# Performance work log

Hardware: AMD Instinct MI355X
Metric: run time of the kernel (lower is better)

Reference implementation:

```python
import jax, jax.numpy as jnp
import numpy as np

CODEBOOK_NUM = 8192
CODEBOOK_DIM = 256
BETA = 1.0


def setup_inputs() -> dict:
    key = jax.random.key(0)
    k1, k2 = jax.random.split(key)
    z = jax.random.normal(k1, (8, CODEBOOK_DIM, 16, 16, 16), dtype=jnp.float32)
    # torch init: uniform_(-1/codebook_num, 1/codebook_num)
    codebook = jax.random.uniform(
        k2, (CODEBOOK_NUM, CODEBOOK_DIM), dtype=jnp.float32,
        minval=-1.0 / CODEBOOK_NUM, maxval=1.0 / CODEBOOK_NUM)
    return {"z": z, "codebook": codebook}


def reference(z, codebook):
    # z: [B, C, D, H, W] -> [B, D, H, W, C]
    zp = jnp.transpose(z, (0, 2, 3, 4, 1))
    z_flat = zp.reshape(-1, codebook.shape[1])  # [N, C]
    # squared euclidean distances via ||a||^2 + ||b||^2 - 2 a.b
    d = (jnp.sum(z_flat ** 2, axis=1, keepdims=True)
         + jnp.sum(codebook ** 2, axis=1)
         - 2.0 * jnp.matmul(z_flat, codebook.T))  # [N, K]
    idx = jnp.argmin(d, axis=1)  # [N]
    z_q = codebook[idx].reshape(zp.shape)  # [B, D, H, W, C]
    sg = jax.lax.stop_gradient
    loss = jnp.mean((sg(z_q) - zp) ** 2) + BETA * jnp.mean((z_q - sg(zp)) ** 2)
    # straight-through estimator
    z_q_st = zp + sg(z_q - zp)
    out = jnp.transpose(z_q_st, (0, 4, 1, 2, 3))  # back to [B, C, D, H, W]
    return out, loss, idx
```

## Files before the change

kernel.cpp:

```cpp
#include <hip/hip_runtime.h>
#include <hip/hip_bf16.h>
#include <stdint.h>
#include <stddef.h>

typedef unsigned short ushort_t;
typedef unsigned int uint_t;

typedef __attribute__((ext_vector_type(8))) short short8;
typedef __attribute__((ext_vector_type(4))) float floatx4;
typedef __attribute__((ext_vector_type(16))) float floatx16;
typedef __attribute__((ext_vector_type(4))) uint_t uintx4;

#define N_ROWS 32768
#define K_ENT  8192
#define CDIM   256
#define OUT_ELEMS 8388608
#define LOSS_OFF  8388608
#define IDX_OFF   8388609
#define CAP_Q  44
#define MARGIN    2.0e-4f

__device__ __forceinline__ ushort_t f2bf(float f) {
    uint_t x = __float_as_uint(f);
    uint_t r = (x + 0x7fffu + ((x >> 16) & 1u)) >> 16;
    return (ushort_t)r;
}


__device__ __forceinline__ void gload_lds16(const ushort_t* g, ushort_t* s) {
    __builtin_amdgcn_global_load_lds(
        (__attribute__((address_space(1))) void*)(g),
        (__attribute__((address_space(3))) void*)(s), 16, 0, 0);
}

__global__ __launch_bounds__(256) void k_prep(const float* __restrict__ zin,
                                              const float* __restrict__ cb,
                                              ushort_t* __restrict__ zsw,
                                              ushort_t* __restrict__ cbsw,
                                              float* __restrict__ ztf,
                                              float* __restrict__ cn) {
    int bid = blockIdx.x;
    if (bid >= 2048) {
        int t = (bid - 2048) * 256 + threadIdx.x;
        int ent = t >> 5;
        int c0  = (t & 31) << 3;
        const float* p = cb + (size_t)ent * CDIM + c0;
        floatx4 f0 = *(const floatx4*)p;
        floatx4 f1 = *(const floatx4*)(p + 4);
        uintx4 pk;
        pk[0] = (uint_t)f2bf(f0[0]) | ((uint_t)f2bf(f0[1]) << 16);
        pk[1] = (uint_t)f2bf(f0[2]) | ((uint_t)f2bf(f0[3]) << 16);
        pk[2] = (uint_t)f2bf(f1[0]) | ((uint_t)f2bf(f1[1]) << 16);
        pk[3] = (uint_t)f2bf(f1[2]) | ((uint_t)f2bf(f1[3]) << 16);
        int idx = (ent >> 5) * 8192 + (c0 >> 4) * 512 + ((c0 >> 3) & 1) * 256 + (ent & 31) * 8;
        *(uintx4*)(cbsw + idx) = pk;
        float pn = 0.f;
#pragma unroll
        for (int qq = 0; qq < 4; ++qq) pn = fmaf(f0[qq], f0[qq], pn);
#pragma unroll
        for (int qq = 0; qq < 4; ++qq) pn = fmaf(f1[qq], f1[qq], pn);
#pragma unroll
        for (int m = 1; m < 32; m <<= 1) pn += __shfl_xor(pn, m);
        if ((t & 31) == 0) cn[ent] = pn;
        return;
    }
    __shared__ float lds[64][65];
    int c0 = (bid & 3) << 6;
    int s0 = ((bid >> 2) & 63) << 6;
    int b  = bid >> 8;
    int tid = threadIdx.x;
    int j = tid & 63, ib = tid >> 6;
    const float* zb = zin + ((size_t)b << 20);
#pragma unroll
    for (int rr = 0; rr < 16; ++rr) {
        int i = rr * 4 + ib;
        lds[i][j] = zb[(size_t)(c0 + i) * 4096 + s0 + j];
    }
    __syncthreads();
#pragma unroll
    for (int it = 0; it < 2; ++it) {
        int item = it * 256 + tid;
        int sl = item >> 3;
        int ch = item & 7;
        int row = (b << 12) + s0 + sl;
        int cg  = c0 + ch * 8;
        uintx4 pk;
        floatx4 f0, f1;
#pragma unroll
        for (int q = 0; q < 4; ++q) {
            float a = lds[ch * 8 + 2 * q][sl];
            float bqv = lds[ch * 8 + 2 * q + 1][sl];
            pk[q] = (uint_t)f2bf(a) | ((uint_t)f2bf(bqv) << 16);
        }
#pragma unroll
        for (int q = 0; q < 4; ++q) {
            f0[q] = lds[ch * 8 + q][sl];
            f1[q] = lds[ch * 8 + 4 + q][sl];
        }
        int idx = (row >> 5) * 8192 + (cg >> 4) * 512 + ((cg >> 3) & 1) * 256 + (row & 31) * 8;
        *(uintx4*)(zsw + idx) = pk;
        if (ztf) {
            *(floatx4*)(ztf + (size_t)row * 256 + cg) = f0;
            *(floatx4*)(ztf + (size_t)row * 256 + cg + 4) = f1;
        }
    }
}

__device__ __forceinline__ void screen_emit(const floatx16& acc, float& rmx,
                                            int& cur, int hi, int2* slist,
                                            int ent0) {
    float t0 = fmaxf(fmaxf(acc[0], acc[1]), fmaxf(acc[2], acc[3]));
    float t1 = fmaxf(fmaxf(acc[4], acc[5]), fmaxf(acc[6], acc[7]));
    float t2 = fmaxf(fmaxf(acc[8], acc[9]), fmaxf(acc[10], acc[11]));
    float t3 = fmaxf(fmaxf(acc[12], acc[13]), fmaxf(acc[14], acc[15]));
    float mxo = fmaxf(fmaxf(t0, t1), fmaxf(t2, t3));
    float mx = fmaxf(mxo, __shfl_xor(mxo, 32));
    float rm = fmaxf(rmx, mx);
    rmx = rm;
    float thr = rm - MARGIN;
    if (__any(mxo >= thr)) {
        uint_t mask = 0u;
#pragma unroll
        for (int r = 0; r < 16; ++r)
            if (acc[r] >= thr) mask |= (1u << r);
        int p  = __popc(mask);
        int pp = __shfl_xor(p, 32);
        int s  = cur + (hi ? pp : 0);
        cur += p + pp;
        if (mask) {
#pragma unroll
            for (int r = 0; r < 16; ++r) {
                if (mask & (1u << r)) {
                    if (s < CAP_Q)
                        slist[s] = make_int2(ent0 + (r & 3) + 8 * (r >> 2),
                                             __float_as_int(acc[r]));
                    ++s;
                }
            }
        }
    }
}

__global__ __launch_bounds__(256, 4) void k_screen(const ushort_t* __restrict__ zsw,
                                                   const ushort_t* __restrict__ cbsw,
                                                   int2* __restrict__ surv,
                                                   int* __restrict__ cnt) {
    __shared__ ushort_t bt[2][8192];
    int tid = threadIdx.x;
    int w = tid >> 6, l = tid & 63;
    int bid = blockIdx.x;
    int q  = bid & 3;
    int RB = (bid >> 2) * 128;
    int n = RB + w * 32 + (l & 31);
    int cidx = n * 4 + q;
    int2* slist = surv + (size_t)cidx * CAP_Q;
    int tile0 = q * 64;
    int hi = l & 32;

    const ushort_t* gsp = cbsw + (size_t)tile0 * 8192 + tid * 8;
    auto stage = [&](ushort_t* ld) {
#pragma unroll
        for (int j = 0; j < 4; ++j)
            gload_lds16(gsp + j * 2048, ld + j * 2048);
        gsp += 8192;
    };

    stage(&bt[0][w * 512]);

    short8 zfr[16];
    {
        const ushort_t* pz = zsw + (size_t)((RB >> 5) + w) * 8192 + l * 8;
#pragma unroll
        for (int s = 0; s < 16; ++s)
            zfr[s] = *(const short8*)(pz + s * 512);
    }
    __syncthreads();

    float rmx = -3.0e38f;
    int cur = 0;
    int esub = (l >> 5) * 4;

    floatx16 zacc;
#pragma unroll
    for (int i = 0; i < 16; ++i) zacc[i] = 0.f;

    floatx16 accA, accB;
    auto compute = [&](floatx16& acc, int b) {
        const ushort_t* bb = &bt[b][l * 8];
        short8 a0 = *(const short8*)(bb);
        acc = __builtin_amdgcn_mfma_f32_32x32x16_bf16(a0, zfr[0], zacc, 0, 0, 0);
#pragma unroll
        for (int s = 1; s < 16; ++s) {
            short8 a = *(const short8*)(bb + s * 512);
            acc = __builtin_amdgcn_mfma_f32_32x32x16_bf16(a, zfr[s], acc, 0, 0, 0);
        }
    };
    auto ent_of = [&](int t) { return (tile0 + t) * 32 + esub; };

    stage(&bt[1][w * 512]);
    __builtin_amdgcn_s_setprio(1);
    compute(accA, 0);
    __builtin_amdgcn_s_setprio(0);
    __syncthreads();

    for (int t = 1; t < 63; t += 2) {
        stage(&bt[0][w * 512]);
        __builtin_amdgcn_s_setprio(1);
        compute(accB, 1);
        screen_emit(accA, rmx, cur, hi, slist, ent_of(t - 1));
        __builtin_amdgcn_s_setprio(0);
        __syncthreads();
        stage(&bt[1][w * 512]);
        __builtin_amdgcn_s_setprio(1);
        compute(accA, 0);
        screen_emit(accB, rmx, cur, hi, slist, ent_of(t));
        __builtin_amdgcn_s_setprio(0);
        __syncthreads();
    }
    __builtin_amdgcn_s_setprio(1);
    compute(accB, 1);
    screen_emit(accA, rmx, cur, hi, slist, ent_of(62));
    __builtin_amdgcn_s_setprio(0);
    screen_emit(accB, rmx, cur, hi, slist, ent_of(63));

    if (!hi) cnt[cidx] = cur;
}

__global__ __launch_bounds__(256) void k_refine(const float* __restrict__ zin,
                                                const float* __restrict__ ztf,
                                                const float* __restrict__ cb,
                                                const int2* __restrict__ surv,
                                                const int* __restrict__ cnt,
                                                int* __restrict__ idxi,
                                                float* __restrict__ idxf,
                                                const float* __restrict__ cn,
                                                float* __restrict__ lossp) {
    __shared__ float zr[4][256];
    __shared__ float lossw[4];
    int w = threadIdx.x >> 6, l = threadIdx.x & 63;
    int n = blockIdx.x * 4 + w;
    if (ztf) {
        const float* zrow = ztf + (size_t)n * 256;
#pragma unroll
        for (int i = 0; i < 4; ++i)
            zr[w][l + 64 * i] = zrow[l + 64 * i];
    } else {
        int b = n >> 12, s = n & 4095;
        const float* zb = zin + ((size_t)b << 20) + s;
#pragma unroll
        for (int i = 0; i < 4; ++i)
            zr[w][l + 64 * i] = zb[(size_t)(l + 64 * i) << 12];
    }
    __syncthreads();
    const float* z = zr[w];
    float zn = 0.f;
    for (int c = 0; c < 256; ++c) zn = fmaf(z[c], z[c], zn);

    int c0 = cnt[n * 4 + 0], c1 = cnt[n * 4 + 1];
    int c2 = cnt[n * 4 + 2], c3 = cnt[n * 4 + 3];
    int m = c0 + c1 + c2 + c3;
    bool ok = (c0 <= CAP_Q) && (c1 <= CAP_Q) && (c2 <= CAP_Q) && (c3 <= CAP_Q) && (m >= 1);
    float bu = 3.0e38f;
    int bk = 0x7fffffff;
    if (ok) {
        int myk[3]; float myv[3]; int nc = 0;
        float vmax = -3.0e38f;
        for (int i = l; i < m; i += 64) {
            int qq, s;
            if (i < c0)            { qq = 0; s = i; }
            else if (i < c0 + c1)  { qq = 1; s = i - c0; }
            else if (i < c0 + c1 + c2) { qq = 2; s = i - c0 - c1; }
            else                   { qq = 3; s = i - c0 - c1 - c2; }
            int2 kv = surv[(n * 4 + qq) * CAP_Q + s];
            myk[nc] = kv.x;
            myv[nc] = __int_as_float(kv.y);
            vmax = fmaxf(vmax, myv[nc]);
            ++nc;
        }
#pragma unroll
        for (int msk = 1; msk < 64; msk <<= 1)
            vmax = fmaxf(vmax, __shfl_xor(vmax, msk));
        float fthr = vmax - MARGIN;
        for (int jj = 0; jj < nc; ++jj) {
            if (myv[jj] >= fthr) {
                int k = myk[jj];
                const float* cr = cb + (size_t)k * 256;
                float d = 0.f;
                for (int c = 0; c < 256; c += 4) {
                    floatx4 wv = *(const floatx4*)(cr + c);
                    d = fmaf(z[c], wv[0], d);
                    d = fmaf(z[c + 1], wv[1], d);
                    d = fmaf(z[c + 2], wv[2], d);
                    d = fmaf(z[c + 3], wv[3], d);
                }
                float u = zn - 2.0f * d;
                if (u < bu || (u == bu && k < bk)) { bu = u; bk = k; }
            }
        }
    } else {
        for (int kb = l; kb < K_ENT; kb += 256) {
            const float* p0 = cb + (size_t)(kb)       * 256;
            const float* p1 = cb + (size_t)(kb + 64)  * 256;
            const float* p2 = cb + (size_t)(kb + 128) * 256;
            const float* p3 = cb + (size_t)(kb + 192) * 256;
            float d0 = 0.f, d1 = 0.f, d2 = 0.f, d3 = 0.f;
            for (int c = 0; c < 256; c += 4) {
                floatx4 w0 = *(const floatx4*)(p0 + c);
                floatx4 w1 = *(const floatx4*)(p1 + c);
                floatx4 w2 = *(const floatx4*)(p2 + c);
                floatx4 w3 = *(const floatx4*)(p3 + c);
#pragma unroll
                for (int j = 0; j < 4; ++j) {
                    d0 = fmaf(z[c + j], w0[j], d0);
                    d1 = fmaf(z[c + j], w1[j], d1);
                    d2 = fmaf(z[c + j], w2[j], d2);
                    d3 = fmaf(z[c + j], w3[j], d3);
                }
            }
            float u0 = zn - 2.0f * d0, u1 = zn - 2.0f * d1;
            float u2 = zn - 2.0f * d2, u3 = zn - 2.0f * d3;
            if (u0 < bu) { bu = u0; bk = kb; }
            if (u1 < bu) { bu = u1; bk = kb + 64; }
            if (u2 < bu) { bu = u2; bk = kb + 128; }
            if (u3 < bu) { bu = u3; bk = kb + 192; }
        }
    }
#pragma unroll
    for (int msk = 1; msk < 64; msk <<= 1) {
        float ou = __shfl_xor(bu, msk);
        int   ok2 = __shfl_xor(bk, msk);
        if (ou < bu || (ou == bu && ok2 < bk)) { bu = ou; bk = ok2; }
    }
    if (l == 0) {
        idxi[n] = bk;
        idxf[n] = (float)bk;
        lossw[w] = bu + cn[bk];
    }
    __syncthreads();
    if (threadIdx.x == 0)
        lossp[blockIdx.x] = (lossw[0] + lossw[1]) + (lossw[2] + lossw[3]);
}

__global__ __launch_bounds__(256) void k_gather(const float* __restrict__ cb,
                                                const int* __restrict__ idxi,
                                                const float* __restrict__ lossp,
                                                float* __restrict__ out) {
    __shared__ float tile[64][65];
    __shared__ int lk[64];
    __shared__ double dsum[4];
    int t = threadIdx.x;
    int blk = blockIdx.x;
    int b = blk >> 6;
    int s0 = (blk & 63) << 6;
    int n0 = (b << 12) + s0;
    if (t < 64) lk[t] = idxi[n0 + t];
    __syncthreads();
    int wv = t >> 6, ln = t & 63;
    float* ob = out + ((size_t)b << 20);
#pragma unroll
    for (int ct = 0; ct < 4; ++ct) {
        int c0 = ct << 6;
#pragma unroll
        for (int i = 0; i < 16; ++i) {
            int sl = (wv << 4) + i;
            tile[sl][ln] = cb[(size_t)lk[sl] * 256 + c0 + ln];
        }
        __syncthreads();
#pragma unroll
        for (int j = 0; j < 16; ++j) {
            int cl = (wv << 4) + j;
            ob[(size_t)(c0 + cl) * 4096 + s0 + ln] = tile[ln][cl];
        }
        __syncthreads();
    }
    if (blk == 0) {
        double s = 0.0;
        for (int i = t; i < 8192; i += 256) s += (double)lossp[i];
#pragma unroll
        for (int msk = 1; msk < 64; msk <<= 1) s += __shfl_xor(s, msk);
        if (ln == 0) dsum[wv] = s;
        __syncthreads();
        if (t == 0)
            out[LOSS_OFF] = (float)(2.0 * ((dsum[0] + dsum[1]) + (dsum[2] + dsum[3]))
                                    / 8388608.0);
    }
}

extern "C" void kernel_launch(void* const* d_in, const int* in_sizes, int n_in,
                              void* d_out, int out_size, void* d_ws, size_t ws_size,
                              hipStream_t stream) {
    (void)in_sizes; (void)n_in; (void)out_size;
    const float* z  = (const float*)d_in[0];
    const float* cb = (const float*)d_in[1];
    float* out = (float*)d_out;
    char* ws = (char*)d_ws;

    size_t off = 0;
    ushort_t* zsw  = (ushort_t*)(ws + off); off += 16777216;
    ushort_t* cbsw = (ushort_t*)(ws + off); off += 4194304;
    float* ztf = nullptr;
    const size_t ZTF_BYTES = 33554432;
    const size_t SURV_BYTES = (size_t)N_ROWS * 4 * CAP_Q * 8;
    const size_t TAIL = SURV_BYTES + 524288 + 131072 + 32768 + 32768;
    if (ws_size >= off + ZTF_BYTES + TAIL) { ztf = (float*)(ws + off); off += ZTF_BYTES; }
    int2* surv = (int2*)(ws + off); off += SURV_BYTES;
    int* cnt    = (int*)(ws + off); off += 524288;
    int* idxi   = (int*)(ws + off); off += 131072;
    float* cn   = (float*)(ws + off); off += 32768;
    float* lossp = (float*)(ws + off); off += 32768;

    k_prep<<<3072, 256, 0, stream>>>(z, cb, zsw, cbsw, ztf, cn);
    k_screen<<<1024, 256, 0, stream>>>(zsw, cbsw, surv, cnt);
    k_refine<<<8192, 256, 0, stream>>>(z, ztf, cb, surv, cnt, idxi, out + IDX_OFF, cn, lossp);
    k_gather<<<8192 / 16, 256, 0, stream>>>(cb, idxi, lossp, out);
}
```

Measured before the change: 336.2 us.

## Fuse refine and gather kernels, drop fp32 transposed z copy

Merges the per-row refine kernel and the gather/transpose kernel into one kernel. Each block loads a 64-row z tile into LDS straight from the NCDHW input, refines those rows, then writes the gathered codebook rows back transposed. The 32 MB fp32 transposed z buffer and the separate index and loss-partial buffers go away. The loss is reduced with double atomics plus a last-block counter instead of a final pass. The risk is lower parallelism in refine: 512 blocks, each running 16 rows serially per wave, instead of 8192 blocks, and any fallback full scan now stalls a whole block.

```diff
diff --git a/kernel.cpp b/kernel.cpp
--- a/kernel.cpp
+++ b/kernel.cpp
@@ -37,11 +37,13 @@
                                               const float* __restrict__ cb,
                                               ushort_t* __restrict__ zsw,
                                               ushort_t* __restrict__ cbsw,
-                                              float* __restrict__ ztf,
-                                              float* __restrict__ cn) {
+                                              float* __restrict__ cn,
+                                              double* __restrict__ acc,
+                                              int* __restrict__ cnt2) {
     int bid = blockIdx.x;
     if (bid >= 2048) {
         int t = (bid - 2048) * 256 + threadIdx.x;
+        if (t == 0) { *acc = 0.0; *cnt2 = 0; }
         int ent = t >> 5;
         int c0  = (t & 31) << 3;
         const float* p = cb + (size_t)ent * CDIM + c0;
@@ -85,24 +87,14 @@
         int row = (b << 12) + s0 + sl;
         int cg  = c0 + ch * 8;
         uintx4 pk;
-        floatx4 f0, f1;
 #pragma unroll
         for (int q = 0; q < 4; ++q) {
             float a = lds[ch * 8 + 2 * q][sl];
             float bqv = lds[ch * 8 + 2 * q + 1][sl];
             pk[q] = (uint_t)f2bf(a) | ((uint_t)f2bf(bqv) << 16);
         }
-#pragma unroll
-        for (int q = 0; q < 4; ++q) {
-            f0[q] = lds[ch * 8 + q][sl];
-            f1[q] = lds[ch * 8 + 4 + q][sl];
-        }
         int idx = (row >> 5) * 8192 + (cg >> 4) * 512 + ((cg >> 3) & 1) * 256 + (row & 31) * 8;
         *(uintx4*)(zsw + idx) = pk;
-        if (ztf) {
-            *(floatx4*)(ztf + (size_t)row * 256 + cg) = f0;
-            *(floatx4*)(ztf + (size_t)row * 256 + cg + 4) = f1;
-        }
     }
 }
 
@@ -226,170 +218,167 @@
     if (!hi) cnt[cidx] = cur;
 }
 
-__global__ __launch_bounds__(256) void k_refine(const float* __restrict__ zin,
-                                                const float* __restrict__ ztf,
+__global__ __launch_bounds__(256) void k_refgat(const float* __restrict__ zin,
                                                 const float* __restrict__ cb,
                                                 const int2* __restrict__ surv,
                                                 const int* __restrict__ cnt,
-                                                int* __restrict__ idxi,
-                                                float* __restrict__ idxf,
                                                 const float* __restrict__ cn,
-                                                float* __restrict__ lossp) {
-    __shared__ float zr[4][256];
+                                                float* __restrict__ out,
+                                                double* __restrict__ acc,
+                                                int* __restrict__ cnt2) {
+    __shared__ float zr[64][257];
+    __shared__ int lk[64];
     __shared__ float lossw[4];
-    int w = threadIdx.x >> 6, l = threadIdx.x & 63;
-    int n = blockIdx.x * 4 + w;
-    if (ztf) {
-        const float* zrow = ztf + (size_t)n * 256;
-#pragma unroll
-        for (int i = 0; i < 4; ++i)
-            zr[w][l + 64 * i] = zrow[l + 64 * i];
-    } else {
-        int b = n >> 12, s = n & 4095;
-        const float* zb = zin + ((size_t)b << 20) + s;
-#pragma unroll
-        for (int i = 0; i < 4; ++i)
-            zr[w][l + 64 * i] = zb[(size_t)(l + 64 * i) << 12];
-    }
-    __syncthreads();
-    const float* z = zr[w];
-    float zn = 0.f;
-    for (int c = 0; c < 256; ++c) zn = fmaf(z[c], z[c], zn);
-
-    int c0 = cnt[n * 4 + 0], c1 = cnt[n * 4 + 1];
-    int c2 = cnt[n * 4 + 2], c3 = cnt[n * 4 + 3];
-    int m = c0 + c1 + c2 + c3;
-    bool ok = (c0 <= CAP_Q) && (c1 <= CAP_Q) && (c2 <= CAP_Q) && (c3 <= CAP_Q) && (m >= 1);
-    float bu = 3.0e38f;
-    int bk = 0x7fffffff;
-    if (ok) {
-        int myk[3]; float myv[3]; int nc = 0;
-        float vmax = -3.0e38f;
-        for (int i = l; i < m; i += 64) {
-            int qq, s;
-            if (i < c0)            { qq = 0; s = i; }
-            else if (i < c0 + c1)  { qq = 1; s = i - c0; }
-            else if (i < c0 + c1 + c2) { qq = 2; s = i - c0 - c1; }
-            else                   { qq = 3; s = i - c0 - c1 - c2; }
-            int2 kv = surv[(n * 4 + qq) * CAP_Q + s];
-            myk[nc] = kv.x;
-            myv[nc] = __int_as_float(kv.y);
-            vmax = fmaxf(vmax, myv[nc]);
-            ++nc;
-        }
-#pragma unroll
-        for (int msk = 1; msk < 64; msk <<= 1)
-            vmax = fmaxf(vmax, __shfl_xor(vmax, msk));
-        float fthr = vmax - MARGIN;
-        for (int jj = 0; jj < nc; ++jj) {
-            if (myv[jj] >= fthr) {
-                int k = myk[jj];
-                const float* cr = cb + (size_t)k * 256;
-                float d = 0.f;
-                for (int c = 0; c < 256; c += 4) {
-                    floatx4 wv = *(const floatx4*)(cr + c);
-                    d = fmaf(z[c], wv[0], d);
-                    d = fmaf(z[c + 1], wv[1], d);
-                    d = fmaf(z[c + 2], wv[2], d);
-                    d = fmaf(z[c + 3], wv[3], d);
-                }
-                float u = zn - 2.0f * d;
-                if (u < bu || (u == bu && k < bk)) { bu = u; bk = k; }
-            }
-        }
-    } else {
-        for (int kb = l; kb < K_ENT; kb += 256) {
-            const float* p0 = cb + (size_t)(kb)       * 256;
-            const float* p1 = cb + (size_t)(kb + 64)  * 256;
-            const float* p2 = cb + (size_t)(kb + 128) * 256;
-            const float* p3 = cb + (size_t)(kb + 192) * 256;
-            float d0 = 0.f, d1 = 0.f, d2 = 0.f, d3 = 0.f;
-            for (int c = 0; c < 256; c += 4) {
-                floatx4 w0 = *(const floatx4*)(p0 + c);
-                floatx4 w1 = *(const floatx4*)(p1 + c);
-                floatx4 w2 = *(const floatx4*)(p2 + c);
-                floatx4 w3 = *(const floatx4*)(p3 + c);
-#pragma unroll
-                for (int j = 0; j < 4; ++j) {
-                    d0 = fmaf(z[c + j], w0[j], d0);
-                    d1 = fmaf(z[c + j], w1[j], d1);
-                    d2 = fmaf(z[c + j], w2[j], d2);
-                    d3 = fmaf(z[c + j], w3[j], d3);
-                }
-            }
-            float u0 = zn - 2.0f * d0, u1 = zn - 2.0f * d1;
-            float u2 = zn - 2.0f * d2, u3 = zn - 2.0f * d3;
-            if (u0 < bu) { bu = u0; bk = kb; }
-            if (u1 < bu) { bu = u1; bk = kb + 64; }
-            if (u2 < bu) { bu = u2; bk = kb + 128; }
-            if (u3 < bu) { bu = u3; bk = kb + 192; }
-        }
-    }
-#pragma unroll
-    for (int msk = 1; msk < 64; msk <<= 1) {
-        float ou = __shfl_xor(bu, msk);
-        int   ok2 = __shfl_xor(bk, msk);
-        if (ou < bu || (ou == bu && ok2 < bk)) { bu = ou; bk = ok2; }
-    }
-    if (l == 0) {
-        idxi[n] = bk;
-        idxf[n] = (float)bk;
-        lossw[w] = bu + cn[bk];
-    }
-    __syncthreads();
-    if (threadIdx.x == 0)
-        lossp[blockIdx.x] = (lossw[0] + lossw[1]) + (lossw[2] + lossw[3]);
-}
-
-__global__ __launch_bounds__(256) void k_gather(const float* __restrict__ cb,
-                                                const int* __restrict__ idxi,
-                                                const float* __restrict__ lossp,
-                                                float* __restrict__ out) {
-    __shared__ float tile[64][65];
-    __shared__ int lk[64];
-    __shared__ double dsum[4];
     int t = threadIdx.x;
+    int wq = t >> 6, l = t & 63;
     int blk = blockIdx.x;
     int b = blk >> 6;
     int s0 = (blk & 63) << 6;
     int n0 = (b << 12) + s0;
-    if (t < 64) lk[t] = idxi[n0 + t];
+    const float* zb = zin + ((size_t)b << 20);
+
+#pragma unroll
+    for (int k = 0; k < 16; ++k) {
+        int item = t + k * 256;
+        int c = item >> 4;
+        int sq = item & 15;
+        floatx4 f = *(const floatx4*)(zb + (size_t)c * 4096 + s0 + sq * 4);
+#pragma unroll
+        for (int j = 0; j < 4; ++j) zr[sq * 4 + j][c] = f[j];
+    }
     __syncthreads();
-    int wv = t >> 6, ln = t & 63;
+
+    float lsum = 0.f;
+    for (int rr = 0; rr < 16; ++rr) {
+        int rl = (wq << 4) + rr;
+        int n = n0 + rl;
+        const float* z = &zr[rl][0];
+        float zn = 0.f;
+#pragma unroll
+        for (int j = 0; j < 4; ++j) { float v = z[l + 64 * j]; zn = fmaf(v, v, zn); }
+#pragma unroll
+        for (int msk = 1; msk < 64; msk <<= 1) zn += __shfl_xor(zn, msk);
+
+        int q0 = cnt[n * 4 + 0], q1 = cnt[n * 4 + 1];
+        int q2 = cnt[n * 4 + 2], q3 = cnt[n * 4 + 3];
+        int m = q0 + q1 + q2 + q3;
+        bool ok = (q0 <= CAP_Q) && (q1 <= CAP_Q) && (q2 <= CAP_Q) && (q3 <= CAP_Q) && (m >= 1);
+        float bu = 3.0e38f;
+        int bk = 0x7fffffff;
+        if (ok) {
+            int myk[3]; float myv[3]; int nc = 0;
+            float vmax = -3.0e38f;
+            for (int i = l; i < m; i += 64) {
+                int qq, s;
+                if (i < q0)                { qq = 0; s = i; }
+                else if (i < q0 + q1)      { qq = 1; s = i - q0; }
+                else if (i < q0 + q1 + q2) { qq = 2; s = i - q0 - q1; }
+                else                       { qq = 3; s = i - q0 - q1 - q2; }
+                int2 kv = surv[(n * 4 + qq) * CAP_Q + s];
+                myk[nc] = kv.x;
+                myv[nc] = __int_as_float(kv.y);
+                vmax = fmaxf(vmax, myv[nc]);
+                ++nc;
+            }
+#pragma unroll
+            for (int msk = 1; msk < 64; msk <<= 1)
+                vmax = fmaxf(vmax, __shfl_xor(vmax, msk));
+            float fthr = vmax - MARGIN;
+            for (int jj = 0; jj < nc; ++jj) {
+                if (myv[jj] >= fthr) {
+                    int k = myk[jj];
+                    const float* cr = cb + (size_t)k * 256;
+                    float d = 0.f;
+                    for (int c = 0; c < 256; c += 4) {
+                        floatx4 cwv = *(const floatx4*)(cr + c);
+                        d = fmaf(z[c], cwv[0], d);
+                        d = fmaf(z[c + 1], cwv[1], d);
+                        d = fmaf(z[c + 2], cwv[2], d);
+                        d = fmaf(z[c + 3], cwv[3], d);
+                    }
+                    float u = zn - 2.0f * d;
+                    if (u < bu || (u == bu && k < bk)) { bu = u; bk = k; }
+                }
+            }
+        } else {
+            for (int kb = l; kb < K_ENT; kb += 256) {
+                const float* p0 = cb + (size_t)(kb)       * 256;
+                const float* p1 = cb + (size_t)(kb + 64)  * 256;
+                const float* p2 = cb + (size_t)(kb + 128) * 256;
+                const float* p3 = cb + (size_t)(kb + 192) * 256;
+                float d0 = 0.f, d1 = 0.f, d2 = 0.f, d3 = 0.f;
+                for (int c = 0; c < 256; c += 4) {
+                    floatx4 w0 = *(const floatx4*)(p0 + c);
+                    floatx4 w1 = *(const floatx4*)(p1 + c);
+                    floatx4 w2 = *(const floatx4*)(p2 + c);
+                    floatx4 w3 = *(const floatx4*)(p3 + c);
+#pragma unroll
+                    for (int j = 0; j < 4; ++j) {
+                        d0 = fmaf(z[c + j], w0[j], d0);
+                        d1 = fmaf(z[c + j], w1[j], d1);
+                        d2 = fmaf(z[c + j], w2[j], d2);
+                        d3 = fmaf(z[c + j], w3[j], d3);
+                    }
+                }
+                float u0 = zn - 2.0f * d0, u1 = zn - 2.0f * d1;
+                float u2 = zn - 2.0f * d2, u3 = zn - 2.0f * d3;
+                if (u0 < bu) { bu = u0; bk = kb; }
+                if (u1 < bu) { bu = u1; bk = kb + 64; }
+                if (u2 < bu) { bu = u2; bk = kb + 128; }
+                if (u3 < bu) { bu = u3; bk = kb + 192; }
+            }
+        }
+#pragma unroll
+        for (int msk = 1; msk < 64; msk <<= 1) {
+            float ou = __shfl_xor(bu, msk);
+            int   ok2 = __shfl_xor(bk, msk);
+            if (ou < bu || (ou == bu && ok2 < bk)) { bu = ou; bk = ok2; }
+        }
+        if (l == 0) {
+            lk[rl] = bk;
+            out[IDX_OFF + n] = (float)bk;
+            lsum += bu + cn[bk];
+        }
+    }
+    if (l == 0) lossw[wq] = lsum;
+    __syncthreads();
+
+    float* tb = &zr[0][0];
     float* ob = out + ((size_t)b << 20);
 #pragma unroll
     for (int ct = 0; ct < 4; ++ct) {
-        int c0 = ct << 6;
+        int cc0 = ct << 6;
 #pragma unroll
         for (int i = 0; i < 16; ++i) {
-            int sl = (wv << 4) + i;
-            tile[sl][ln] = cb[(size_t)lk[sl] * 256 + c0 + ln];
+            int sl = (wq << 4) + i;
+            tb[sl * 65 + l] = cb[(size_t)lk[sl] * 256 + cc0 + l];
         }
         __syncthreads();
 #pragma unroll
         for (int j = 0; j < 16; ++j) {
-            int cl = (wv << 4) + j;
-            ob[(size_t)(c0 + cl) * 4096 + s0 + ln] = tile[ln][cl];
+            int cl = (wq << 4) + j;
+            ob[(size_t)(cc0 + cl) * 4096 + s0 + l] = tb[l * 65 + cl];
         }
         __syncthreads();
     }
-    if (blk == 0) {
-        double s = 0.0;
-        for (int i = t; i < 8192; i += 256) s += (double)lossp[i];
-#pragma unroll
-        for (int msk = 1; msk < 64; msk <<= 1) s += __shfl_xor(s, msk);
-        if (ln == 0) dsum[wv] = s;
-        __syncthreads();
-        if (t == 0)
-            out[LOSS_OFF] = (float)(2.0 * ((dsum[0] + dsum[1]) + (dsum[2] + dsum[3]))
-                                    / 8388608.0);
+
+    if (t == 0) {
+        float tot = (lossw[0] + lossw[1]) + (lossw[2] + lossw[3]);
+        atomicAdd(acc, (double)tot);
+        __threadfence();
+        int done = atomicAdd(cnt2, 1);
+        if (done == (int)gridDim.x - 1) {
+            __threadfence();
+            double v = atomicAdd(acc, 0.0);
+            out[LOSS_OFF] = (float)(2.0 * v / 8388608.0);
+        }
     }
 }
 
 extern "C" void kernel_launch(void* const* d_in, const int* in_sizes, int n_in,
                               void* d_out, int out_size, void* d_ws, size_t ws_size,
                               hipStream_t stream) {
-    (void)in_sizes; (void)n_in; (void)out_size;
+    (void)in_sizes; (void)n_in; (void)out_size; (void)ws_size;
     const float* z  = (const float*)d_in[0];
     const float* cb = (const float*)d_in[1];
     float* out = (float*)d_out;
@@ -398,19 +387,14 @@
     size_t off = 0;
     ushort_t* zsw  = (ushort_t*)(ws + off); off += 16777216;
     ushort_t* cbsw = (ushort_t*)(ws + off); off += 4194304;
-    float* ztf = nullptr;
-    const size_t ZTF_BYTES = 33554432;
     const size_t SURV_BYTES = (size_t)N_ROWS * 4 * CAP_Q * 8;
-    const size_t TAIL = SURV_BYTES + 524288 + 131072 + 32768 + 32768;
-    if (ws_size >= off + ZTF_BYTES + TAIL) { ztf = (float*)(ws + off); off += ZTF_BYTES; }
     int2* surv = (int2*)(ws + off); off += SURV_BYTES;
     int* cnt    = (int*)(ws + off); off += 524288;
-    int* idxi   = (int*)(ws + off); off += 131072;
     float* cn   = (float*)(ws + off); off += 32768;
-    float* lossp = (float*)(ws + off); off += 32768;
-
-    k_prep<<<3072, 256, 0, stream>>>(z, cb, zsw, cbsw, ztf, cn);
+    double* acc = (double*)(ws + off); off += 8;
+    int* cnt2   = (int*)(ws + off);
+
+    k_prep<<<3072, 256, 0, stream>>>(z, cb, zsw, cbsw, cn, acc, cnt2);
     k_screen<<<1024, 256, 0, stream>>>(zsw, cbsw, surv, cnt);
-    k_refine<<<8192, 256, 0, stream>>>(z, ztf, cb, surv, cnt, idxi, out + IDX_OFF, cn, lossp);
-    k_gather<<<8192 / 16, 256, 0, stream>>>(cb, idxi, lossp, out);
-}
+    k_refgat<<<512, 256, 0, stream>>>(z, cb, surv, cnt, cn, out, acc, cnt2);
+}
```

Result: slower. 346.7 us (+3.1%).
